# Kernel optimization log

Measured on AMD Instinct MI355X. Metric: run time of the kernel, lower is better.

Reference implementation:

```python
import jax, jax.numpy as jnp
import numpy as np

# Constants describing the (equal-length) ragged batch and CRF tag space
B, L = 64, 512                 # 64 sequences of 512 segment-tokens each
C = 1024                       # fuse_embedding_channel
NUM_CLASSES = 5                # real field classes
NUM_TAGS = NUM_CLASSES + 2     # + START + STOP
START, STOP = NUM_CLASSES, NUM_CLASSES + 1
NEG = -10000.0


def setup_inputs() -> dict:
    key = jax.random.key(0)
    k1, k2, k3, k4 = jax.random.split(key, 4)
    fuse_embeddings = jax.random.normal(k1, (B * L, C), jnp.float32)
    label_class = jax.random.randint(k2, (B * L,), 0, NUM_CLASSES)
    # classification head params (Linear C -> NUM_TAGS)
    W = jax.random.normal(k3, (NUM_TAGS, C), jnp.float32) * 0.02
    b = jnp.zeros((NUM_TAGS,), jnp.float32)
    # CRF transition matrix: transitions[next, prev]
    transitions = jax.random.normal(k4, (NUM_TAGS, NUM_TAGS), jnp.float32) * 0.01
    transitions = transitions.at[START, :].set(NEG).at[:, STOP].set(NEG)
    return {"fuse_embeddings": fuse_embeddings, "label_class": label_class,
            "W": W, "b": b, "transitions": transitions}


def _crf_nll_sum(feats, tags, transitions):
    """Sum over batch of (forward_alg score - gold score).
    feats: [B, L, T] emissions, tags: [B, L] int, transitions: [T, T] (next, prev)."""
    # --- forward algorithm (batched log-sum-exp recurrence) ---
    init = jnp.full((B, NUM_TAGS), NEG, feats.dtype).at[:, START].set(0.0)

    def step(fv, emit):
        # fv: [B, prev], emit: [B, next]
        fv_new = jax.nn.logsumexp(fv[:, None, :] + transitions[None, :, :], axis=2) + emit
        return fv_new, None

    fv, _ = jax.lax.scan(step, init, jnp.swapaxes(feats, 0, 1))  # scan over L
    fwd_score = jax.nn.logsumexp(fv + transitions[STOP][None, :], axis=1)  # [B]

    # --- gold sentence score ---
    tags_ext = jnp.concatenate([jnp.full((B, 1), START, tags.dtype), tags], axis=1)
    emit_sc = jnp.take_along_axis(feats, tags[..., None], axis=2)[..., 0].sum(axis=1)
    trans_sc = transitions[tags_ext[:, 1:], tags_ext[:, :-1]].sum(axis=1)
    gold = emit_sc + trans_sc + transitions[STOP, tags[:, -1]]
    return (fwd_score - gold).sum()


def reference(fuse_embeddings, label_class, W, b, transitions):
    # per-token linear projection to tag logits
    pred_class = fuse_embeddings @ W.T + b          # [N, NUM_TAGS]
    feats = pred_class.reshape(B, L, NUM_TAGS)
    tags = label_class.reshape(B, L)
    score = _crf_nll_sum(feats, tags, transitions)
    return (jnp.reshape(score, (1,)), label_class.astype(jnp.int32), pred_class)
```

## Files before the change

kernel.cpp:

```cpp
#include <hip/hip_runtime.h>

#define BSEQ 64
#define LSEQ 512
#define CCH  1024
#define NT   7
#define NC   5
#define NTOK (BSEQ*LSEQ)
#define START_TAG 5
#define STOP_TAG  6
#define NEGV (-10000.0f)
#define GRID_LOGITS 1024

typedef float vfloat4 __attribute__((ext_vector_type(4)));

template<int CTRL, int RMASK, int BMASK>
__device__ __forceinline__ float dpp_add(float x) {
    int y = __builtin_amdgcn_update_dpp(0, __float_as_int(x), CTRL, RMASK, BMASK, true);
    return x + __int_as_float(y);
}
__device__ __forceinline__ float wave_sum(float x) {
    x = dpp_add<0x111, 0xF, 0xF>(x);
    x = dpp_add<0x112, 0xF, 0xF>(x);
    x = dpp_add<0x114, 0xF, 0xF>(x);
    x = dpp_add<0x118, 0xF, 0xF>(x);
    x = dpp_add<0x142, 0xA, 0xF>(x);
    x = dpp_add<0x143, 0xC, 0xF>(x);
    return x;
}

__device__ __forceinline__ float lse5(const float v0, const float v1, const float v2,
                                      const float v3, const float v4) {
    float m = fmaxf(fmaxf(fmaxf(v0, v1), fmaxf(v2, v3)), v4);
    float s = __expf(v0 - m) + __expf(v1 - m) + __expf(v2 - m)
            + __expf(v3 - m) + __expf(v4 - m);
    return m + __logf(s);
}

__global__ __launch_bounds__(256)
void k_logits(const float* __restrict__ X, const float* __restrict__ W,
              const float* __restrict__ bvec, const int* __restrict__ lab,
              float* __restrict__ out)
{
    __shared__ float Wl[NT][CCH];
    __shared__ float bl[NT];

    const int lane = threadIdx.x & 63;
    const int wid  = (blockIdx.x * 256 + threadIdx.x) >> 6;
    const int nw   = (GRID_LOGITS * 256) >> 6;

    vfloat4 xv[5][4];

    #pragma unroll
    for (int p = 0; p < 4; p++) {
        const vfloat4* xr = (const vfloat4*)(X + (size_t)(wid + p * nw) * CCH);
        #pragma unroll
        for (int k = 0; k < 4; k++) xv[p][k] = xr[k*64 + lane];
    }

    {
        const vfloat4* W4  = (const vfloat4*)W;
        vfloat4*       Wl4 = (vfloat4*)(&Wl[0][0]);
        for (int i = threadIdx.x; i < NT*CCH/4; i += 256) Wl4[i] = W4[i];
        if (threadIdx.x < NT) bl[threadIdx.x] = bvec[threadIdx.x];
    }
    __syncthreads();

    float* outP = out + 1 + NTOK;

    #pragma unroll
    for (int it = 0; it < 8; ++it) {
        const int buf = it % 5;
        if (it < 4) {
            const vfloat4* xr = (const vfloat4*)(X + (size_t)(wid + (it + 4) * nw) * CCH);
            const int nb = (it + 4) % 5;
            #pragma unroll
            for (int k = 0; k < 4; k++) xv[nb][k] = xr[k*64 + lane];
        }

        float acc[NT];
        #pragma unroll
        for (int t = 0; t < NT; t++) acc[t] = 0.0f;

        #pragma unroll
        for (int k = 0; k < 4; k++) {
            const int cb = (k*64 + lane) * 4;
            #pragma unroll
            for (int t = 0; t < NT; t++) {
                const vfloat4 wv = *(const vfloat4*)(&Wl[t][cb]);
                acc[t] = fmaf(xv[buf][k].x, wv.x,
                         fmaf(xv[buf][k].y, wv.y,
                         fmaf(xv[buf][k].z, wv.z,
                         fmaf(xv[buf][k].w, wv.w, acc[t]))));
            }
        }

        const size_t row = (size_t)(wid + it * nw);
        #pragma unroll
        for (int t = 0; t < NT; t++) {
            float s = wave_sum(acc[t]);
            if (lane == 63) outP[row * NT + t] = s + bl[t];
        }
    }

    for (int i = blockIdx.x * 256 + threadIdx.x; i < NTOK; i += GRID_LOGITS * 256)
        out[1 + i] = (float)lab[i];
    if (blockIdx.x == 0 && threadIdx.x == 0) out[0] = 0.0f;
}

__global__ __launch_bounds__(320)
void k_crf(const float* __restrict__ dout_ro, const int* __restrict__ lab,
           const float* __restrict__ trans, float* __restrict__ score)
{
    __shared__ float E[LSEQ*NT];
    __shared__ float M2[32*25];
    __shared__ float T[49];
    __shared__ float u_sh[NC];
    __shared__ float gred[5];

    const int b   = blockIdx.x;
    const int tid = threadIdx.x;
    const float* feats = dout_ro + 1 + NTOK + (size_t)b * (LSEQ*NT);

    for (int i = tid; i < LSEQ*NT; i += 320) E[i] = feats[i];
    if (tid < 49) T[tid] = trans[tid];
    __syncthreads();

    if (tid < NC) u_sh[tid] = T[tid*NT + START_TAG] + E[tid];

    float g = 0.0f;
    for (int l = tid; l < LSEQ; l += 320) {
        const int t  = lab[b*LSEQ + l];
        const int tp = (l == 0) ? START_TAG : lab[b*LSEQ + l - 1];
        g += E[l*NT + t] + T[t*NT + tp];
    }
    if (tid == 0) g += T[STOP_TAG*NT + lab[b*LSEQ + LSEQ - 1]];
    {
        float gs = wave_sum(g);
        if ((tid & 63) == 63) gred[tid >> 6] = gs;
    }

    float TR[NC*NC];
    #pragma unroll
    for (int j = 0; j < NC; j++)
        #pragma unroll
        for (int k = 0; k < NC; k++) TR[j*NC + k] = T[j*NT + k];

    const int chunk = tid / NC;
    const int basis = tid - chunk * NC;
    float fv[NC];
    #pragma unroll
    for (int j = 0; j < NC; j++) fv[j] = (j == basis) ? 0.0f : NEGV;

    const int l0    = (chunk == 0) ? 1 : chunk * 8;
    const int steps = (chunk == 0) ? 7 : 8;
    for (int s = 0; s < steps; s++) {
        const int l = l0 + s;
        float fn[NC];
        #pragma unroll
        for (int j = 0; j < NC; j++) {
            fn[j] = lse5(fv[0] + TR[j*NC+0], fv[1] + TR[j*NC+1], fv[2] + TR[j*NC+2],
                         fv[3] + TR[j*NC+3], fv[4] + TR[j*NC+4]) + E[l*NT + j];
        }
        #pragma unroll
        for (int j = 0; j < NC; j++) fv[j] = fn[j];
    }
    __syncthreads();
    #pragma unroll
    for (int j = 0; j < NC; j++) E[chunk*25 + basis*NC + j] = fv[j];

    int n = 64, cur = 0;
    while (n > 1) {
        __syncthreads();
        const float* in = (cur == 0) ? (const float*)E : (const float*)M2;
        float*       ob = (cur == 0) ? M2 : E;
        const int half = n >> 1;
        for (int e2 = tid; e2 < half*25; e2 += 320) {
            const int p = e2 / 25, r = e2 - p*25;
            const int i = r / NC, j = r - (r/NC)*NC;
            const float* A  = in + (2*p)*25 + i*NC;
            const float* Bm = in + (2*p + 1)*25 + j;
            ob[p*25 + r] = lse5(A[0] + Bm[0], A[1] + Bm[NC], A[2] + Bm[2*NC],
                                A[3] + Bm[3*NC], A[4] + Bm[4*NC]);
        }
        cur ^= 1; n = half;
    }
    __syncthreads();

    if (tid == 0) {
        float gg = gred[0] + gred[1] + gred[2] + gred[3] + gred[4];
        const float* M = (cur == 0) ? (const float*)E : (const float*)M2;
        float v[NC];
        #pragma unroll
        for (int j = 0; j < NC; j++)
            v[j] = lse5(u_sh[0] + M[0*NC+j], u_sh[1] + M[1*NC+j], u_sh[2] + M[2*NC+j],
                        u_sh[3] + M[3*NC+j], u_sh[4] + M[4*NC+j]);
        float fwd = lse5(v[0] + T[STOP_TAG*NT+0], v[1] + T[STOP_TAG*NT+1],
                         v[2] + T[STOP_TAG*NT+2], v[3] + T[STOP_TAG*NT+3],
                         v[4] + T[STOP_TAG*NT+4]);
        atomicAdd(score, fwd - gg);
    }
}

extern "C" void kernel_launch(void* const* d_in, const int* in_sizes, int n_in,
                              void* d_out, int out_size, void* d_ws, size_t ws_size,
                              hipStream_t stream) {
    const float* X     = (const float*)d_in[0];
    const int*   lab   = (const int*)  d_in[1];
    const float* W     = (const float*)d_in[2];
    const float* bvec  = (const float*)d_in[3];
    const float* trans = (const float*)d_in[4];
    float* out = (float*)d_out;

    k_logits<<<GRID_LOGITS, 256, 0, stream>>>(X, W, bvec, lab, out);
    k_crf<<<BSEQ, 320, 0, stream>>>(out, lab, trans, out);
}
```

Baseline: 218.7 us.

## Process four rows per phase to reuse LDS weight loads, with nontemporal loads

The logits kernel now works on groups of four rows per wave and walks the channel chunks phase by phase. Each phase loads the 7 weight vectors from LDS once and reuses them across four rows, instead of reloading them for every row. X loads become nontemporal, and the prefetch depth drops from five buffers to a three-slot ring, two phases ahead. The goal is to cut LDS traffic and register pressure while keeping the streaming loads of X in flight. The trade-offs are 28 accumulators held live and a shallower prefetch that may expose more memory latency.

Result: faster. 214.0 us (-2.1%).

```diff
diff --git a/kernel.cpp b/kernel.cpp
--- a/kernel.cpp
+++ b/kernel.cpp
@@ -48,14 +48,21 @@
     const int wid  = (blockIdx.x * 256 + threadIdx.x) >> 6;
     const int nw   = (GRID_LOGITS * 256) >> 6;
 
-    vfloat4 xv[5][4];
-
-    #pragma unroll
-    for (int p = 0; p < 4; p++) {
-        const vfloat4* xr = (const vfloat4*)(X + (size_t)(wid + p * nw) * CCH);
-        #pragma unroll
-        for (int k = 0; k < 4; k++) xv[p][k] = xr[k*64 + lane];
-    }
+    vfloat4 xb[3][4];
+
+    #define ISSUE_PHASE(p, slot)                                                   \
+        if ((p) < 8) {                                                             \
+            const int G_ = (p) >> 2, k_ = (p) & 3;                                 \
+            _Pragma("unroll")                                                      \
+            for (int j = 0; j < 4; j++) {                                          \
+                const size_t row_ = (size_t)(wid + (G_*4 + j) * nw);               \
+                const vfloat4* xp_ = (const vfloat4*)(X + row_ * CCH) + (k_*64 + lane); \
+                xb[slot][j] = __builtin_nontemporal_load(xp_);                     \
+            }                                                                      \
+        }
+
+    ISSUE_PHASE(0, 0)
+    ISSUE_PHASE(1, 1)
 
     {
         const vfloat4* W4  = (const vfloat4*)W;
@@ -67,40 +74,53 @@
 
     float* outP = out + 1 + NTOK;
 
-    #pragma unroll
-    for (int it = 0; it < 8; ++it) {
-        const int buf = it % 5;
-        if (it < 4) {
-            const vfloat4* xr = (const vfloat4*)(X + (size_t)(wid + (it + 4) * nw) * CCH);
-            const int nb = (it + 4) % 5;
-            #pragma unroll
-            for (int k = 0; k < 4; k++) xv[nb][k] = xr[k*64 + lane];
-        }
-
-        float acc[NT];
-        #pragma unroll
-        for (int t = 0; t < NT; t++) acc[t] = 0.0f;
-
-        #pragma unroll
-        for (int k = 0; k < 4; k++) {
+    float acc[4][NT];
+    #pragma unroll
+    for (int j = 0; j < 4; j++)
+        #pragma unroll
+        for (int t = 0; t < NT; t++) acc[j][t] = 0.0f;
+
+    #pragma unroll
+    for (int p = 0; p < 8; ++p) {
+        const int slot = p % 3;
+        const int k    = p & 3;
+
+        ISSUE_PHASE(p + 2, (p + 2) % 3)
+
+        vfloat4 wreg[NT];
+        {
             const int cb = (k*64 + lane) * 4;
             #pragma unroll
+            for (int t = 0; t < NT; t++)
+                wreg[t] = *(const vfloat4*)(&Wl[t][cb]);
+        }
+
+        #pragma unroll
+        for (int j = 0; j < 4; j++) {
+            #pragma unroll
             for (int t = 0; t < NT; t++) {
-                const vfloat4 wv = *(const vfloat4*)(&Wl[t][cb]);
-                acc[t] = fmaf(xv[buf][k].x, wv.x,
-                         fmaf(xv[buf][k].y, wv.y,
-                         fmaf(xv[buf][k].z, wv.z,
-                         fmaf(xv[buf][k].w, wv.w, acc[t]))));
+                acc[j][t] = fmaf(xb[slot][j].x, wreg[t].x,
+                            fmaf(xb[slot][j].y, wreg[t].y,
+                            fmaf(xb[slot][j].z, wreg[t].z,
+                            fmaf(xb[slot][j].w, wreg[t].w, acc[j][t]))));
             }
         }
 
-        const size_t row = (size_t)(wid + it * nw);
-        #pragma unroll
-        for (int t = 0; t < NT; t++) {
-            float s = wave_sum(acc[t]);
-            if (lane == 63) outP[row * NT + t] = s + bl[t];
-        }
-    }
+        if (k == 3) {
+            const int G = p >> 2;
+            #pragma unroll
+            for (int j = 0; j < 4; j++) {
+                const size_t row = (size_t)(wid + (G*4 + j) * nw);
+                #pragma unroll
+                for (int t = 0; t < NT; t++) {
+                    float s = wave_sum(acc[j][t]);
+                    if (lane == 63) outP[row * NT + t] = s + bl[t];
+                    acc[j][t] = 0.0f;
+                }
+            }
+        }
+    }
+    #undef ISSUE_PHASE
 
     for (int i = blockIdx.x * 256 + threadIdx.x; i < NTOK; i += GRID_LOGITS * 256)
         out[1 + i] = (float)lab[i];
```
